# Optimization experiments

Measured on AMD Instinct MI355X. Metric: run time of the kernel, lower is better.

## Reference

```python
import jax, jax.numpy as jnp
import numpy as np

# Static config (matches init_kwargs / spatial layout)
SHAPES = ((64, 64), (32, 32), (16, 16))   # (H, W) per level, bev=256 at /4,/8,/16
B, HEADS, LEVELS, POINTS, C = 2, 8, 3, 4, 256
HD = C // HEADS
NV = sum(h * w for h, w in SHAPES)        # 5376
NQ = NV
TP = HEADS * LEVELS * POINTS              # 96


def setup_inputs() -> dict:
    key = jax.random.key(0)
    ks = jax.random.split(key, 10)
    s = 1.0 / np.sqrt(C)
    inp = {
        'query': jax.random.normal(ks[0], (B, NQ, C), dtype=jnp.float32),
        'reference_points': jax.random.uniform(ks[1], (B, NQ, 2), dtype=jnp.float32),
        'value': jax.random.normal(ks[2], (B, NV, C), dtype=jnp.float32),
        'Wv': jax.random.normal(ks[3], (C, C), dtype=jnp.float32) * s,
        'bv': jnp.zeros((C,), dtype=jnp.float32),
        # offset proj: small scale so sampling stays local-ish (orig init is 0)
        'Woff': jax.random.normal(ks[4], (TP * 2, C), dtype=jnp.float32) * (0.02 * s),
        'boff': jnp.zeros((TP * 2,), dtype=jnp.float32),
        'Wa': jax.random.normal(ks[5], (TP, C), dtype=jnp.float32) * s,
        'ba': jnp.zeros((TP,), dtype=jnp.float32),
        'Wo': jax.random.normal(ks[6], (C, C), dtype=jnp.float32) * s,
        'bo': jnp.zeros((C,), dtype=jnp.float32),
    }
    return inp


def _msda(query, reference_points, value, Wv, bv, Woff, boff, Wa, ba, Wo, bo):
    Bb, nq, _ = query.shape
    # value projection -> per-head values
    v = (value @ Wv.T + bv).reshape(Bb, NV, HEADS, HD)
    # sampling offsets: (B, NQ, HEADS, LEVELS, POINTS, 2)
    off = (query @ Woff.T + boff).reshape(Bb, nq, HEADS, LEVELS, POINTS, 2)
    # attention weights: softmax over LEVELS*POINTS jointly
    a = (query @ Wa.T + ba).reshape(Bb, nq, HEADS, LEVELS * POINTS)
    a = jax.nn.softmax(a, axis=-1).reshape(Bb, nq, HEADS, LEVELS, POINTS)
    # sampling locations in [0,1] (clamp matches torch .clamp(0,1))
    loc = jnp.clip(reference_points[:, :, None, None, None, :] + off, 0.0, 1.0)

    out = jnp.zeros((Bb, HEADS, nq, HD), dtype=query.dtype)
    start = 0
    for lvl, (H, W) in enumerate(SHAPES):
        n = H * W
        # (B, HEADS, H*W, HD) flattened level feature map per head
        vl = jnp.transpose(v[:, start:start + n].reshape(Bb, H, W, HEADS, HD),
                           (0, 3, 1, 2, 4)).reshape(Bb, HEADS, n, HD)
        loc_l = loc[:, :, :, lvl]                     # (B, NQ, HEADS, K, 2)
        # align_corners=False unnormalization: ((g+1)*size - 1)/2 with g=2*loc-1
        x = loc_l[..., 0] * W - 0.5
        y = loc_l[..., 1] * H - 0.5
        x0 = jnp.floor(x)
        y0 = jnp.floor(y)
        wx1 = x - x0
        wy1 = y - y0
        x0i = x0.astype(jnp.int32)
        y0i = y0.astype(jnp.int32)
        acc = jnp.zeros((Bb, HEADS, nq * POINTS, HD), dtype=query.dtype)
        for dy in (0, 1):
            for dx in (0, 1):
                ix = x0i + dx
                iy = y0i + dy
                wgt = (wx1 if dx else 1.0 - wx1) * (wy1 if dy else 1.0 - wy1)
                # zero padding outside the map (padding_mode='zeros')
                valid = (ix >= 0) & (ix < W) & (iy >= 0) & (iy < H)
                idx = jnp.clip(iy, 0, H - 1) * W + jnp.clip(ix, 0, W - 1)
                idx_t = jnp.transpose(idx, (0, 2, 1, 3)).reshape(Bb, HEADS, nq * POINTS)
                g = jnp.take_along_axis(vl, idx_t[..., None], axis=2)  # (B,H,NQ*K,HD)
                w_t = jnp.transpose(wgt * valid.astype(wgt.dtype),
                                    (0, 2, 1, 3)).reshape(Bb, HEADS, nq * POINTS, 1)
                acc = acc + g * w_t
        aw = jnp.transpose(a[:, :, :, lvl], (0, 2, 1, 3)).reshape(Bb, HEADS, nq * POINTS, 1)
        out = out + (acc * aw).reshape(Bb, HEADS, nq, POINTS, HD).sum(axis=3)
        start += n
    out = jnp.transpose(out, (0, 2, 1, 3)).reshape(Bb, nq, C)
    return out @ Wo.T + bo


def reference(query, reference_points, value, Wv, bv, Woff, boff, Wa, ba, Wo, bo):
    return _msda(query, reference_points, value, Wv, bv, Woff, boff, Wa, ba, Wo, bo)
```

## Files before the change

kernel.cpp:

```cpp
#include <hip/hip_runtime.h>
#include <hip/hip_bf16.h>
#include <cmath>

#define BATCH   2
#define NQ      5376
#define NV      5376
#define CDIM    256
#define HEADS   8
#define HD      32
#define LEVELS  3
#define POINTS  4
#define TP      96
#define MROWS   (BATCH*NQ)
#define NOFF    (TP*2)
#define NQA     (NOFF+TP)

typedef __attribute__((ext_vector_type(8))) short bf16x8;
typedef __attribute__((ext_vector_type(4))) float f32x4;
typedef unsigned short u16;
typedef unsigned int   u32;

#define AS1 __attribute__((address_space(1)))
#define AS3 __attribute__((address_space(3)))

__device__ __forceinline__ void g2lds16(const void* g, void* l) {
    __builtin_amdgcn_global_load_lds((const AS1 void*)g, (AS3 void*)l, 16, 0, 0);
}

__device__ __forceinline__ u16 bf_of(float f) {
    union { __hip_bfloat16 h; u16 s; } u;
    u.h = __float2bfloat16(f);
    return u.s;
}
__device__ __forceinline__ float bf_back(u16 s) {
    return __uint_as_float((u32)s << 16);
}

__device__ __forceinline__ ushort4 cvt_hi(float4 v) {
    ushort4 h;
    h.x = bf_of(v.x); h.y = bf_of(v.y); h.z = bf_of(v.z); h.w = bf_of(v.w);
    return h;
}
__device__ __forceinline__ ushort4 cvt_lo(float4 v, ushort4 h) {
    ushort4 l;
    l.x = bf_of(v.x - bf_back(h.x));
    l.y = bf_of(v.y - bf_back(h.y));
    l.z = bf_of(v.z - bf_back(h.z));
    l.w = bf_of(v.w - bf_back(h.w));
    return l;
}

#define GBM 64
#define GBN 64
#define GBK 32

#define VBLOCKS (168 * 4)
__global__ __launch_bounds__(256) void gemm_vqa_kernel(
    const float* __restrict__ value, const float* __restrict__ Wv,
    const float* __restrict__ bv, u16* __restrict__ vOut,
    const float* __restrict__ query, const float* __restrict__ Woff,
    const float* __restrict__ Wa,
    const float* __restrict__ boff, const float* __restrict__ ba,
    u16* __restrict__ offOut, u16* __restrict__ aOut)
{
    __shared__ u16 sAh[GBM * GBK];
    __shared__ u16 sAl[GBM * GBK];
    __shared__ u16 sBh[GBN * GBK];

    const int bid = blockIdx.x;
    const bool vpath = bid < VBLOCKS;
    int m0, n0;
    if (vpath) { m0 = (bid >> 2) * GBM;           n0 = (bid & 3) * GBN; }
    else       { const int b2 = bid - VBLOCKS;
                 m0 = (b2 / 5) * GBM;             n0 = (b2 % 5) * GBN; }

    const int tid  = threadIdx.x;
    const int lane = tid & 63;
    const int wave = tid >> 6;
    const int wr   = wave & 1;
    const int wc   = wave >> 1;
    const int qm   = lane & 15;
    const int quad = lane >> 4;

    const int srow = tid >> 2;
    const int sc   = (tid & 3) * 8;

    const float* Asrc = (vpath ? value : query) + (size_t)(m0 + srow) * CDIM;
    const float* Bsrc;
    if (vpath) {
        Bsrc = Wv + (size_t)(n0 + srow) * CDIM;
    } else {
        const int rg = min(n0 + srow, NQA - 1);
        Bsrc = (rg < NOFF) ? (Woff + (size_t)rg * CDIM)
                           : (Wa + (size_t)(rg - NOFF) * CDIM);
    }

    f32x4 acc[2][2];
    #pragma unroll
    for (int i = 0; i < 2; ++i)
        #pragma unroll
        for (int j = 0; j < 2; ++j)
            acc[i][j] = (f32x4){0.f, 0.f, 0.f, 0.f};

    for (int k0 = 0; k0 < CDIM; k0 += GBK) {
        const float4 a0 = *reinterpret_cast<const float4*>(&Asrc[k0 + sc]);
        const float4 a1 = *reinterpret_cast<const float4*>(&Asrc[k0 + sc + 4]);
        const ushort4 ah0 = cvt_hi(a0), ah1 = cvt_hi(a1);
        *reinterpret_cast<ushort4*>(&sAh[srow * GBK + sc])     = ah0;
        *reinterpret_cast<ushort4*>(&sAh[srow * GBK + sc + 4]) = ah1;
        if (vpath) {
            *reinterpret_cast<ushort4*>(&sAl[srow * GBK + sc])     = cvt_lo(a0, ah0);
            *reinterpret_cast<ushort4*>(&sAl[srow * GBK + sc + 4]) = cvt_lo(a1, ah1);
        }
        const float4 b0 = *reinterpret_cast<const float4*>(&Bsrc[k0 + sc]);
        const float4 b1 = *reinterpret_cast<const float4*>(&Bsrc[k0 + sc + 4]);
        *reinterpret_cast<ushort4*>(&sBh[srow * GBK + sc])     = cvt_hi(b0);
        *reinterpret_cast<ushort4*>(&sBh[srow * GBK + sc + 4]) = cvt_hi(b1);
        __syncthreads();

        bf16x8 fah[2], fal[2], fbh[2];
        #pragma unroll
        for (int x = 0; x < 2; ++x) {
            const int rm = wr * 32 + x * 16 + qm;
            const int rn = wc * 32 + x * 16 + qm;
            fah[x] = *reinterpret_cast<const bf16x8*>(&sAh[rm * GBK + quad * 8]);
            fbh[x] = *reinterpret_cast<const bf16x8*>(&sBh[rn * GBK + quad * 8]);
            if (vpath)
                fal[x] = *reinterpret_cast<const bf16x8*>(&sAl[rm * GBK + quad * 8]);
        }
        #pragma unroll
        for (int mi = 0; mi < 2; ++mi)
            #pragma unroll
            for (int ni = 0; ni < 2; ++ni) {
                acc[mi][ni] = __builtin_amdgcn_mfma_f32_16x16x32_bf16(
                    fah[mi], fbh[ni], acc[mi][ni], 0, 0, 0);
                if (vpath)
                    acc[mi][ni] = __builtin_amdgcn_mfma_f32_16x16x32_bf16(
                        fal[mi], fbh[ni], acc[mi][ni], 0, 0, 0);
            }
        __syncthreads();
    }

    #pragma unroll
    for (int mi = 0; mi < 2; ++mi) {
        #pragma unroll
        for (int ni = 0; ni < 2; ++ni) {
            const int n = n0 + wc * 32 + ni * 16 + qm;
            if (vpath) {
                const float bn = bv[n];
                #pragma unroll
                for (int r = 0; r < 4; ++r) {
                    const int m = m0 + wr * 32 + mi * 16 + quad * 4 + r;
                    const float val = acc[mi][ni][r] + bn;
                    const int b = m / NV, rr = m - b * NV;
                    const int h = n >> 5, c = n & 31;
                    vOut[(((size_t)b * HEADS + h) * NV + rr) * HD + c] = bf_of(val);
                }
            } else {
                if (n >= NQA) continue;
                const float bn = (n < NOFF) ? boff[n] : ba[n - NOFF];
                #pragma unroll
                for (int r = 0; r < 4; ++r) {
                    const int m = m0 + wr * 32 + mi * 16 + quad * 4 + r;
                    const float val = acc[mi][ni][r] + bn;
                    if (n < NOFF)
                        offOut[(size_t)m * NOFF + n] = bf_of(val);
                    else
                        aOut[(size_t)m * TP + (n - NOFF)] = bf_of(val);
                }
            }
        }
    }
}

__global__ __launch_bounds__(256) void gemm_out_kernel(
    const u16* __restrict__ Ah,
    const float* __restrict__ Wo, const float* __restrict__ bias,
    float* __restrict__ Cout)
{
    __shared__ u16 sAh[GBM * GBK];
    __shared__ u16 sBh[GBN * GBK];

    const int bid = blockIdx.x;
    const int m0 = (bid >> 2) * GBM;
    const int n0 = (bid & 3) * GBN;

    const int tid  = threadIdx.x;
    const int lane = tid & 63;
    const int wave = tid >> 6;
    const int wr   = wave & 1;
    const int wc   = wave >> 1;
    const int qm   = lane & 15;
    const int quad = lane >> 4;

    const int arow = (wave << 4) + (lane >> 2);
    const int ak   = (lane & 3) * 8;
    const int srow = tid >> 2;
    const int sc   = (tid & 3) * 8;
    const float* Bsrc = Wo + (size_t)(n0 + srow) * CDIM;

    f32x4 acc[2][2];
    #pragma unroll
    for (int i = 0; i < 2; ++i)
        #pragma unroll
        for (int j = 0; j < 2; ++j)
            acc[i][j] = (f32x4){0.f, 0.f, 0.f, 0.f};

    for (int k0 = 0; k0 < CDIM; k0 += GBK) {
        const size_t ga = (size_t)(m0 + arow) * CDIM + k0 + ak;
        g2lds16(Ah + ga, sAh + wave * 512);
        const float4 b0 = *reinterpret_cast<const float4*>(&Bsrc[k0 + sc]);
        const float4 b1 = *reinterpret_cast<const float4*>(&Bsrc[k0 + sc + 4]);
        *reinterpret_cast<ushort4*>(&sBh[srow * GBK + sc])     = cvt_hi(b0);
        *reinterpret_cast<ushort4*>(&sBh[srow * GBK + sc + 4]) = cvt_hi(b1);
        __syncthreads();

        bf16x8 fah[2], fbh[2];
        #pragma unroll
        for (int x = 0; x < 2; ++x) {
            const int rm = wr * 32 + x * 16 + qm;
            const int rn = wc * 32 + x * 16 + qm;
            fah[x] = *reinterpret_cast<const bf16x8*>(&sAh[rm * GBK + quad * 8]);
            fbh[x] = *reinterpret_cast<const bf16x8*>(&sBh[rn * GBK + quad * 8]);
        }
        #pragma unroll
        for (int mi = 0; mi < 2; ++mi)
            #pragma unroll
            for (int ni = 0; ni < 2; ++ni)
                acc[mi][ni] = __builtin_amdgcn_mfma_f32_16x16x32_bf16(
                    fah[mi], fbh[ni], acc[mi][ni], 0, 0, 0);
        __syncthreads();
    }

    #pragma unroll
    for (int mi = 0; mi < 2; ++mi) {
        #pragma unroll
        for (int ni = 0; ni < 2; ++ni) {
            const int n = n0 + wc * 32 + ni * 16 + qm;
            const float bn = bias[n];
            #pragma unroll
            for (int r = 0; r < 4; ++r) {
                const int m = m0 + wr * 32 + mi * 16 + quad * 4 + r;
                Cout[(size_t)m * CDIM + n] = acc[mi][ni][r] + bn;
            }
        }
    }
}

__global__ __launch_bounds__(256) void msda_core_kernel(
    const u16* __restrict__ off,
    const u16* __restrict__ alog,
    const float* __restrict__ refp,
    const u16*   __restrict__ v,
    u16* __restrict__ t_hi)
{
    const int tid = threadIdx.x;
    const int bq0 = blockIdx.x * 4;

    __shared__ float s_w[4][TP];
    __shared__ int   s_idx[4][TP][4];
    __shared__ float s_twt[4][TP][4];

    #pragma unroll
    for (int base = 0; base < 4 * TP; base += 256) {
        const int idx = base + tid;
        if (idx < 4 * TP) {
            const int q = idx / TP, j = idx - q * TP;
            s_w[q][j] = bf_back(alog[(size_t)(bq0 + q) * TP + j]);
        }
    }
    __syncthreads();

    if (tid < 32) {
        const int q = tid >> 3, h = tid & 7;
        float mx = -1e30f;
        #pragma unroll
        for (int i = 0; i < 12; ++i) mx = fmaxf(mx, s_w[q][h * 12 + i]);
        float e[12];
        float sum = 0.f;
        #pragma unroll
        for (int i = 0; i < 12; ++i) {
            e[i] = expf(s_w[q][h * 12 + i] - mx);
            sum += e[i];
        }
        const float inv = 1.f / sum;
        #pragma unroll
        for (int i = 0; i < 12; ++i) s_w[q][h * 12 + i] = e[i] * inv;
    }
    __syncthreads();

    #pragma unroll
    for (int base = 0; base < 4 * TP; base += 256) {
        const int idx = base + tid;
        if (idx < 4 * TP) {
            const int q = idx / TP, j = idx - q * TP;
            const int bq = bq0 + q;
            const int jj = j % 12;
            const int l  = jj >> 2;
            const int Wl    = (l == 0) ? 64 : (l == 1) ? 32 : 16;
            const int start = (l == 0) ? 0 : (l == 1) ? 4096 : 5120;

            const float refx = refp[(size_t)bq * 2 + 0];
            const float refy = refp[(size_t)bq * 2 + 1];
            const float ox = bf_back(off[(size_t)bq * NOFF + j * 2 + 0]);
            const float oy = bf_back(off[(size_t)bq * NOFF + j * 2 + 1]);
            const float lx = fminf(fmaxf(refx + ox, 0.f), 1.f) * (float)Wl - 0.5f;
            const float ly = fminf(fmaxf(refy + oy, 0.f), 1.f) * (float)Wl - 0.5f;
            const float fx0 = floorf(lx), fy0 = floorf(ly);
            const int   x0  = (int)fx0,   y0  = (int)fy0;
            const float wx1 = lx - fx0,   wy1 = ly - fy0;
            const float wx0 = 1.f - wx1,  wy0 = 1.f - wy1;
            const float aw  = s_w[q][j];

            #pragma unroll
            for (int k = 0; k < 4; ++k) {
                const int dx = k & 1, dy = k >> 1;
                const int xi = x0 + dx, yi = y0 + dy;
                const bool ok = (xi >= 0) & (xi < Wl) & (yi >= 0) & (yi < Wl);
                const int xc = min(max(xi, 0), Wl - 1);
                const int yc = min(max(yi, 0), Wl - 1);
                s_idx[q][j][k] = (start + yc * Wl + xc) * (HD * 2);
                const float wxy = (dx ? wx1 : wx0) * (dy ? wy1 : wy0);
                s_twt[q][j][k] = ok ? aw * wxy : 0.f;
            }
        }
    }
    __syncthreads();

    const int qsel = tid >> 6;
    const int ht   = tid & 63;
    const int h    = ht >> 3;
    const int sub  = ht & 7;
    const int oct  = sub & 3;
    const int rep  = sub >> 2;
    const int bq   = bq0 + qsel;
    const int b    = bq / NQ;
    const char* vb = (const char*)v + (((size_t)b * HEADS + h) * NV) * (HD * 2) + oct * 16;

    float acc[8] = {};
    #pragma unroll
    for (int g = 0; g < 3; ++g) {
        uint4 raw[8];
        float wt[8];
        #pragma unroll
        for (int pp = 0; pp < 2; ++pp) {
            const int j = h * 12 + rep * 6 + g * 2 + pp;
            const int4   ix = *reinterpret_cast<const int4*>(&s_idx[qsel][j][0]);
            const float4 tw = *reinterpret_cast<const float4*>(&s_twt[qsel][j][0]);
            raw[pp * 4 + 0] = *reinterpret_cast<const uint4*>(vb + ix.x);
            raw[pp * 4 + 1] = *reinterpret_cast<const uint4*>(vb + ix.y);
            raw[pp * 4 + 2] = *reinterpret_cast<const uint4*>(vb + ix.z);
            raw[pp * 4 + 3] = *reinterpret_cast<const uint4*>(vb + ix.w);
            wt[pp * 4 + 0] = tw.x; wt[pp * 4 + 1] = tw.y;
            wt[pp * 4 + 2] = tw.z; wt[pp * 4 + 3] = tw.w;
        }
        #pragma unroll
        for (int k = 0; k < 8; ++k) {
            acc[0] += wt[k] * __uint_as_float(raw[k].x << 16);
            acc[1] += wt[k] * __uint_as_float(raw[k].x & 0xffff0000u);
            acc[2] += wt[k] * __uint_as_float(raw[k].y << 16);
            acc[3] += wt[k] * __uint_as_float(raw[k].y & 0xffff0000u);
            acc[4] += wt[k] * __uint_as_float(raw[k].z << 16);
            acc[5] += wt[k] * __uint_as_float(raw[k].z & 0xffff0000u);
            acc[6] += wt[k] * __uint_as_float(raw[k].w << 16);
            acc[7] += wt[k] * __uint_as_float(raw[k].w & 0xffff0000u);
        }
    }

    #pragma unroll
    for (int c = 0; c < 8; ++c)
        acc[c] += __shfl_xor(acc[c], 4);

    if (rep == 0) {
        uint4 o;
        o.x = (u32)bf_of(acc[0]) | ((u32)bf_of(acc[1]) << 16);
        o.y = (u32)bf_of(acc[2]) | ((u32)bf_of(acc[3]) << 16);
        o.z = (u32)bf_of(acc[4]) | ((u32)bf_of(acc[5]) << 16);
        o.w = (u32)bf_of(acc[6]) | ((u32)bf_of(acc[7]) << 16);
        const size_t base = (size_t)bq * CDIM + h * HD + oct * 8;
        *reinterpret_cast<uint4*>(t_hi + base) = o;
    }
}

extern "C" void kernel_launch(void* const* d_in, const int* in_sizes, int n_in,
                              void* d_out, int out_size, void* d_ws, size_t ws_size,
                              hipStream_t stream)
{
    const float* query = (const float*)d_in[0];
    const float* refp  = (const float*)d_in[1];
    const float* value = (const float*)d_in[2];
    const float* Wv    = (const float*)d_in[3];
    const float* bv    = (const float*)d_in[4];
    const float* Woff  = (const float*)d_in[5];
    const float* boff  = (const float*)d_in[6];
    const float* Wa    = (const float*)d_in[7];
    const float* ba    = (const float*)d_in[8];
    const float* Wo    = (const float*)d_in[9];
    const float* bo    = (const float*)d_in[10];
    float* out = (float*)d_out;

    char* w = (char*)d_ws;
    const size_t SZ_T = (size_t)MROWS * CDIM * 2;
    u16* v_bf16 = (u16*)(w);
    u16* t_hi   = (u16*)(w + 1 * SZ_T);
    u16* ws_off = (u16*)(w + 2 * SZ_T);
    u16* ws_a   = (u16*)(w + 2 * SZ_T + (size_t)MROWS * NOFF * 2);

    const dim3 blk(256);

    gemm_vqa_kernel<<<dim3(VBLOCKS + (MROWS / GBM) * 5), blk, 0, stream>>>(
        value, Wv, bv, v_bf16,
        query, Woff, Wa, boff, ba, ws_off, ws_a);

    msda_core_kernel<<<dim3(MROWS / 4), blk, 0, stream>>>(
        ws_off, ws_a, refp, v_bf16, t_hi);

    gemm_out_kernel<<<dim3((MROWS / GBM) * 4), blk, 0, stream>>>(
        t_hi, Wo, bo, out);
}
```

Before: 135.0 us.

## Pre-convert inputs to bf16 and double-buffer GEMM tiles via direct LDS loads

Adds a prep kernel that converts value (hi/lo split), query and all weight matrices to bf16 in the workspace, and pads the combined offset/attention weight to 320 rows. Both GEMM kernels then load tiles with global_load_lds into double-buffered shared memory, prefetching the next K slice while computing the current one. Block indices are also remapped across 8 groups, apparently to spread work across the chip's XCDs. This removes in-loop fp32 conversion and one barrier per K step, at the cost of an extra launch and a full extra pass writing and re-reading the bf16 copies of value and query.

Result: no change. 134.4 us (-0.4%).

```diff
diff --git a/kernel.cpp b/kernel.cpp
--- a/kernel.cpp
+++ b/kernel.cpp
@@ -14,6 +14,7 @@
 #define MROWS   (BATCH*NQ)
 #define NOFF    (TP*2)
 #define NQA     (NOFF+TP)
+#define NQAP    320
 
 typedef __attribute__((ext_vector_type(8))) short bf16x8;
 typedef __attribute__((ext_vector_type(4))) float f32x4;
@@ -50,29 +51,110 @@
     return l;
 }
 
+#define NVAL8  344064
+#define NQRY8  344064
+#define NWV8   8192
+#define NWOFF8 6144
+#define NWA8   3072
+#define NWO8   8192
+#define NPAD8  1024
+#define PREP_BLOCKS 2792
+__global__ __launch_bounds__(256) void prep_kernel(
+    const float* __restrict__ value, const float* __restrict__ query,
+    const float* __restrict__ Wv, const float* __restrict__ Woff,
+    const float* __restrict__ Wa, const float* __restrict__ Wo,
+    u16* __restrict__ val_hi, u16* __restrict__ val_lo,
+    u16* __restrict__ q_hi, u16* __restrict__ wv_h,
+    u16* __restrict__ wqa_h, u16* __restrict__ wo_h)
+{
+    int r = blockIdx.x * 256 + threadIdx.x;
+
+    if (r < NVAL8) {
+        const float4 a0 = *reinterpret_cast<const float4*>(value + (size_t)r * 8);
+        const float4 a1 = *reinterpret_cast<const float4*>(value + (size_t)r * 8 + 4);
+        const ushort4 h0 = cvt_hi(a0), h1 = cvt_hi(a1);
+        *reinterpret_cast<ushort4*>(val_hi + (size_t)r * 8)     = h0;
+        *reinterpret_cast<ushort4*>(val_hi + (size_t)r * 8 + 4) = h1;
+        *reinterpret_cast<ushort4*>(val_lo + (size_t)r * 8)     = cvt_lo(a0, h0);
+        *reinterpret_cast<ushort4*>(val_lo + (size_t)r * 8 + 4) = cvt_lo(a1, h1);
+        return;
+    }
+    r -= NVAL8;
+    if (r < NQRY8) {
+        const float4 a0 = *reinterpret_cast<const float4*>(query + (size_t)r * 8);
+        const float4 a1 = *reinterpret_cast<const float4*>(query + (size_t)r * 8 + 4);
+        *reinterpret_cast<ushort4*>(q_hi + (size_t)r * 8)     = cvt_hi(a0);
+        *reinterpret_cast<ushort4*>(q_hi + (size_t)r * 8 + 4) = cvt_hi(a1);
+        return;
+    }
+    r -= NQRY8;
+    if (r < NWV8) {
+        const float4 a0 = *reinterpret_cast<const float4*>(Wv + (size_t)r * 8);
+        const float4 a1 = *reinterpret_cast<const float4*>(Wv + (size_t)r * 8 + 4);
+        *reinterpret_cast<ushort4*>(wv_h + (size_t)r * 8)     = cvt_hi(a0);
+        *reinterpret_cast<ushort4*>(wv_h + (size_t)r * 8 + 4) = cvt_hi(a1);
+        return;
+    }
+    r -= NWV8;
+    if (r < NWOFF8) {
+        const float4 a0 = *reinterpret_cast<const float4*>(Woff + (size_t)r * 8);
+        const float4 a1 = *reinterpret_cast<const float4*>(Woff + (size_t)r * 8 + 4);
+        *reinterpret_cast<ushort4*>(wqa_h + (size_t)r * 8)     = cvt_hi(a0);
+        *reinterpret_cast<ushort4*>(wqa_h + (size_t)r * 8 + 4) = cvt_hi(a1);
+        return;
+    }
+    r -= NWOFF8;
+    if (r < NWA8) {
+        const float4 a0 = *reinterpret_cast<const float4*>(Wa + (size_t)r * 8);
+        const float4 a1 = *reinterpret_cast<const float4*>(Wa + (size_t)r * 8 + 4);
+        u16* dst = wqa_h + (size_t)NOFF * CDIM;
+        *reinterpret_cast<ushort4*>(dst + (size_t)r * 8)     = cvt_hi(a0);
+        *reinterpret_cast<ushort4*>(dst + (size_t)r * 8 + 4) = cvt_hi(a1);
+        return;
+    }
+    r -= NWA8;
+    if (r < NWO8) {
+        const float4 a0 = *reinterpret_cast<const float4*>(Wo + (size_t)r * 8);
+        const float4 a1 = *reinterpret_cast<const float4*>(Wo + (size_t)r * 8 + 4);
+        *reinterpret_cast<ushort4*>(wo_h + (size_t)r * 8)     = cvt_hi(a0);
+        *reinterpret_cast<ushort4*>(wo_h + (size_t)r * 8 + 4) = cvt_hi(a1);
+        return;
+    }
+    r -= NWO8;
+    const ushort4 z = {0, 0, 0, 0};
+    u16* dst = wqa_h + (size_t)NQA * CDIM;
+    *reinterpret_cast<ushort4*>(dst + (size_t)r * 8)     = z;
+    *reinterpret_cast<ushort4*>(dst + (size_t)r * 8 + 4) = z;
+}
+
 #define GBM 64
 #define GBN 64
 #define GBK 32
 
 #define VBLOCKS (168 * 4)
+#define K1_BLOCKS (VBLOCKS + 168 * 5)
+#define K1_CPX (K1_BLOCKS / 8)
+
 __global__ __launch_bounds__(256) void gemm_vqa_kernel(
-    const float* __restrict__ value, const float* __restrict__ Wv,
-    const float* __restrict__ bv, u16* __restrict__ vOut,
-    const float* __restrict__ query, const float* __restrict__ Woff,
-    const float* __restrict__ Wa,
-    const float* __restrict__ boff, const float* __restrict__ ba,
-    u16* __restrict__ offOut, u16* __restrict__ aOut)
+    const u16* __restrict__ val_hi, const u16* __restrict__ val_lo,
+    const u16* __restrict__ q_hi,
+    const u16* __restrict__ wv_h, const u16* __restrict__ wqa_h,
+    const float* __restrict__ bv, const float* __restrict__ boff,
+    const float* __restrict__ ba,
+    u16* __restrict__ vOut, u16* __restrict__ offOut, u16* __restrict__ aOut)
 {
-    __shared__ u16 sAh[GBM * GBK];
-    __shared__ u16 sAl[GBM * GBK];
-    __shared__ u16 sBh[GBN * GBK];
-
-    const int bid = blockIdx.x;
+    __shared__ __align__(16) u16 sAh[2][GBM * GBK];
+    __shared__ __align__(16) u16 sAl[2][GBM * GBK];
+    __shared__ __align__(16) u16 sBh[2][GBM * GBK];
+
+    const int bid0 = blockIdx.x;
+    const int bid = (bid0 & 7) * K1_CPX + (bid0 >> 3);
+
     const bool vpath = bid < VBLOCKS;
     int m0, n0;
-    if (vpath) { m0 = (bid >> 2) * GBM;           n0 = (bid & 3) * GBN; }
+    if (vpath) { m0 = (bid >> 2) * GBM;          n0 = (bid & 3) * GBM; }
     else       { const int b2 = bid - VBLOCKS;
-                 m0 = (b2 / 5) * GBM;             n0 = (b2 % 5) * GBN; }
+                 m0 = (b2 / 5) * GBM;            n0 = (b2 % 5) * GBM; }
 
     const int tid  = threadIdx.x;
     const int lane = tid & 63;
@@ -82,18 +164,12 @@
     const int qm   = lane & 15;
     const int quad = lane >> 4;
 
-    const int srow = tid >> 2;
-    const int sc   = (tid & 3) * 8;
-
-    const float* Asrc = (vpath ? value : query) + (size_t)(m0 + srow) * CDIM;
-    const float* Bsrc;
-    if (vpath) {
-        Bsrc = Wv + (size_t)(n0 + srow) * CDIM;
-    } else {
-        const int rg = min(n0 + srow, NQA - 1);
-        Bsrc = (rg < NOFF) ? (Woff + (size_t)rg * CDIM)
-                           : (Wa + (size_t)(rg - NOFF) * CDIM);
-    }
+    const int arow = (wave << 4) + (lane >> 2);
+    const int ak   = (lane & 3) * 8;
+
+    const u16* Asrc_h = (vpath ? val_hi : q_hi) + (size_t)(m0 + arow) * CDIM + ak;
+    const u16* Asrc_l = val_lo + (size_t)(m0 + arow) * CDIM + ak;
+    const u16* Bsrc   = (vpath ? wv_h : wqa_h) + (size_t)(n0 + arow) * CDIM + ak;
 
     f32x4 acc[2][2];
     #pragma unroll
@@ -102,31 +178,30 @@
         for (int j = 0; j < 2; ++j)
             acc[i][j] = (f32x4){0.f, 0.f, 0.f, 0.f};
 
+    {
+        g2lds16(Asrc_h, &sAh[0][wave * 512]);
+        if (vpath) g2lds16(Asrc_l, &sAl[0][wave * 512]);
+        g2lds16(Bsrc, &sBh[0][wave * 512]);
+    }
+    __syncthreads();
+
+    int cur = 0;
     for (int k0 = 0; k0 < CDIM; k0 += GBK) {
-        const float4 a0 = *reinterpret_cast<const float4*>(&Asrc[k0 + sc]);
-        const float4 a1 = *reinterpret_cast<const float4*>(&Asrc[k0 + sc + 4]);
-        const ushort4 ah0 = cvt_hi(a0), ah1 = cvt_hi(a1);
-        *reinterpret_cast<ushort4*>(&sAh[srow * GBK + sc])     = ah0;
-        *reinterpret_cast<ushort4*>(&sAh[srow * GBK + sc + 4]) = ah1;
-        if (vpath) {
-            *reinterpret_cast<ushort4*>(&sAl[srow * GBK + sc])     = cvt_lo(a0, ah0);
-            *reinterpret_cast<ushort4*>(&sAl[srow * GBK + sc + 4]) = cvt_lo(a1, ah1);
-        }
-        const float4 b0 = *reinterpret_cast<const float4*>(&Bsrc[k0 + sc]);
-        const float4 b1 = *reinterpret_cast<const float4*>(&Bsrc[k0 + sc + 4]);
-        *reinterpret_cast<ushort4*>(&sBh[srow * GBK + sc])     = cvt_hi(b0);
-        *reinterpret_cast<ushort4*>(&sBh[srow * GBK + sc + 4]) = cvt_hi(b1);
-        __syncthreads();
+        if (k0 + GBK < CDIM) {
+            g2lds16(Asrc_h + k0 + GBK, &sAh[cur ^ 1][wave * 512]);
+            if (vpath) g2lds16(Asrc_l + k0 + GBK, &sAl[cur ^ 1][wave * 512]);
+            g2lds16(Bsrc + k0 + GBK, &sBh[cur ^ 1][wave * 512]);
+        }
 
         bf16x8 fah[2], fal[2], fbh[2];
         #pragma unroll
         for (int x = 0; x < 2; ++x) {
             const int rm = wr * 32 + x * 16 + qm;
             const int rn = wc * 32 + x * 16 + qm;
-            fah[x] = *reinterpret_cast<const bf16x8*>(&sAh[rm * GBK + quad * 8]);
-            fbh[x] = *reinterpret_cast<const bf16x8*>(&sBh[rn * GBK + quad * 8]);
+            fah[x] = *reinterpret_cast<const bf16x8*>(&sAh[cur][rm * GBK + quad * 8]);
+            fbh[x] = *reinterpret_cast<const bf16x8*>(&sBh[cur][rn * GBK + quad * 8]);
             if (vpath)
-                fal[x] = *reinterpret_cast<const bf16x8*>(&sAl[rm * GBK + quad * 8]);
+                fal[x] = *reinterpret_cast<const bf16x8*>(&sAl[cur][rm * GBK + quad * 8]);
         }
         #pragma unroll
         for (int mi = 0; mi < 2; ++mi)
@@ -139,6 +214,7 @@
                         fal[mi], fbh[ni], acc[mi][ni], 0, 0, 0);
             }
         __syncthreads();
+        cur ^= 1;
     }
 
     #pragma unroll
@@ -173,17 +249,20 @@
     }
 }
 
+#define K3_BLOCKS ((MROWS / GBM) * 4)
+#define K3_CPX (K3_BLOCKS / 8)
+
 __global__ __launch_bounds__(256) void gemm_out_kernel(
-    const u16* __restrict__ Ah,
-    const float* __restrict__ Wo, const float* __restrict__ bias,
-    float* __restrict__ Cout)
+    const u16* __restrict__ Ah, const u16* __restrict__ wo_h,
+    const float* __restrict__ bias, float* __restrict__ Cout)
 {
-    __shared__ u16 sAh[GBM * GBK];
-    __shared__ u16 sBh[GBN * GBK];
-
-    const int bid = blockIdx.x;
+    __shared__ __align__(16) u16 sAh[2][GBM * GBK];
+    __shared__ __align__(16) u16 sBh[2][GBM * GBK];
+
+    const int bid0 = blockIdx.x;
+    const int bid = (bid0 & 7) * K3_CPX + (bid0 >> 3);
     const int m0 = (bid >> 2) * GBM;
-    const int n0 = (bid & 3) * GBN;
+    const int n0 = (bid & 3) * GBM;
 
     const int tid  = threadIdx.x;
     const int lane = tid & 63;
@@ -195,9 +274,9 @@
 
     const int arow = (wave << 4) + (lane >> 2);
     const int ak   = (lane & 3) * 8;
-    const int srow = tid >> 2;
-    const int sc   = (tid & 3) * 8;
-    const float* Bsrc = Wo + (size_t)(n0 + srow) * CDIM;
+
+    const u16* Asrc = Ah   + (size_t)(m0 + arow) * CDIM + ak;
+    const u16* Bsrc = wo_h + (size_t)(n0 + arow) * CDIM + ak;
 
     f32x4 acc[2][2];
     #pragma unroll
@@ -206,22 +285,24 @@
         for (int j = 0; j < 2; ++j)
             acc[i][j] = (f32x4){0.f, 0.f, 0.f, 0.f};
 
+    g2lds16(Asrc, &sAh[0][wave * 512]);
+    g2lds16(Bsrc, &sBh[0][wave * 512]);
+    __syncthreads();
+
+    int cur = 0;
     for (int k0 = 0; k0 < CDIM; k0 += GBK) {
-        const size_t ga = (size_t)(m0 + arow) * CDIM + k0 + ak;
-        g2lds16(Ah + ga, sAh + wave * 512);
-        const float4 b0 = *reinterpret_cast<const float4*>(&Bsrc[k0 + sc]);
-        const float4 b1 = *reinterpret_cast<const float4*>(&Bsrc[k0 + sc + 4]);
-        *reinterpret_cast<ushort4*>(&sBh[srow * GBK + sc])     = cvt_hi(b0);
-        *reinterpret_cast<ushort4*>(&sBh[srow * GBK + sc + 4]) = cvt_hi(b1);
-        __syncthreads();
+        if (k0 + GBK < CDIM) {
+            g2lds16(Asrc + k0 + GBK, &sAh[cur ^ 1][wave * 512]);
+            g2lds16(Bsrc + k0 + GBK, &sBh[cur ^ 1][wave * 512]);
+        }
 
         bf16x8 fah[2], fbh[2];
         #pragma unroll
         for (int x = 0; x < 2; ++x) {
             const int rm = wr * 32 + x * 16 + qm;
             const int rn = wc * 32 + x * 16 + qm;
-            fah[x] = *reinterpret_cast<const bf16x8*>(&sAh[rm * GBK + quad * 8]);
-            fbh[x] = *reinterpret_cast<const bf16x8*>(&sBh[rn * GBK + quad * 8]);
+            fah[x] = *reinterpret_cast<const bf16x8*>(&sAh[cur][rm * GBK + quad * 8]);
+            fbh[x] = *reinterpret_cast<const bf16x8*>(&sBh[cur][rn * GBK + quad * 8]);
         }
         #pragma unroll
         for (int mi = 0; mi < 2; ++mi)
@@ -230,6 +311,7 @@
                 acc[mi][ni] = __builtin_amdgcn_mfma_f32_16x16x32_bf16(
                     fah[mi], fbh[ni], acc[mi][ni], 0, 0, 0);
         __syncthreads();
+        cur ^= 1;
     }
 
     #pragma unroll
@@ -405,16 +487,28 @@
     u16* t_hi   = (u16*)(w + 1 * SZ_T);
     u16* ws_off = (u16*)(w + 2 * SZ_T);
     u16* ws_a   = (u16*)(w + 2 * SZ_T + (size_t)MROWS * NOFF * 2);
+    char* w2    = w + 2 * SZ_T + (size_t)MROWS * NQA * 2;
+    u16* val_hi = (u16*)(w2);
+    u16* val_lo = (u16*)(w2 + 1 * SZ_T);
+    u16* q_hi   = (u16*)(w2 + 2 * SZ_T);
+    u16* wv_h   = (u16*)(w2 + 3 * SZ_T);
+    u16* wqa_h  = (u16*)(w2 + 3 * SZ_T + (size_t)CDIM * CDIM * 2);
+    u16* wo_h   = (u16*)(w2 + 3 * SZ_T + (size_t)CDIM * CDIM * 2
+                              + (size_t)NQAP * CDIM * 2);
 
     const dim3 blk(256);
 
-    gemm_vqa_kernel<<<dim3(VBLOCKS + (MROWS / GBM) * 5), blk, 0, stream>>>(
-        value, Wv, bv, v_bf16,
-        query, Woff, Wa, boff, ba, ws_off, ws_a);
+    prep_kernel<<<dim3(PREP_BLOCKS), blk, 0, stream>>>(
+        value, query, Wv, Woff, Wa, Wo,
+        val_hi, val_lo, q_hi, wv_h, wqa_h, wo_h);
+
+    gemm_vqa_kernel<<<dim3(K1_BLOCKS), blk, 0, stream>>>(
+        val_hi, val_lo, q_hi, wv_h, wqa_h,
+        bv, boff, ba, v_bf16, ws_off, ws_a);
 
     msda_core_kernel<<<dim3(MROWS / 4), blk, 0, stream>>>(
         ws_off, ws_a, refp, v_bf16, t_hi);
 
-    gemm_out_kernel<<<dim3((MROWS / GBM) * 4), blk, 0, stream>>>(
-        t_hi, Wo, bo, out);
-}
+    gemm_out_kernel<<<dim3(K3_BLOCKS), blk, 0, stream>>>(
+        t_hi, wo_h, bo, out);
+}
```

## Fuse output projection into MSDA sampling kernel and pre-convert Wo to bf16

Applied to the files above, without the earlier changes.

Merges the sampling/aggregation kernel with the output projection GEMM. Each 512-thread block handles 16 queries, stages the aggregated rows in LDS, and multiplies them by a bf16 copy of Wo using MFMA. This removes the intermediate write and read of the aggregated tensor and one kernel launch. The first kernel also converts Wo to bf16, pads its LDS rows to avoid bank conflicts, and swizzles block indices across XCDs. Softmax is computed per wave, with normalization applied after accumulation. In exchange, the fused kernel uses larger blocks with more LDS, and Wo is reread from global/L2 by every block.

After: 131.5 us. 1.03x faster.

```diff
diff --git a/kernel.cpp b/kernel.cpp
--- a/kernel.cpp
+++ b/kernel.cpp
@@ -20,13 +20,6 @@
 typedef unsigned short u16;
 typedef unsigned int   u32;
 
-#define AS1 __attribute__((address_space(1)))
-#define AS3 __attribute__((address_space(3)))
-
-__device__ __forceinline__ void g2lds16(const void* g, void* l) {
-    __builtin_amdgcn_global_load_lds((const AS1 void*)g, (AS3 void*)l, 16, 0, 0);
-}
-
 __device__ __forceinline__ u16 bf_of(float f) {
     union { __hip_bfloat16 h; u16 s; } u;
     u.h = __float2bfloat16(f);
@@ -35,7 +28,6 @@
 __device__ __forceinline__ float bf_back(u16 s) {
     return __uint_as_float((u32)s << 16);
 }
-
 __device__ __forceinline__ ushort4 cvt_hi(float4 v) {
     ushort4 h;
     h.x = bf_of(v.x); h.y = bf_of(v.y); h.z = bf_of(v.z); h.w = bf_of(v.w);
@@ -53,28 +45,44 @@
 #define GBM 64
 #define GBN 64
 #define GBK 32
+#define SAP 40
 
 #define VBLOCKS (168 * 4)
-__global__ __launch_bounds__(256) void gemm_vqa_kernel(
+#define K1_BLOCKS (VBLOCKS + 168 * 5)
+#define K1_CPX (K1_BLOCKS / 8)
+
+__global__ __launch_bounds__(256) void gemm_vqa_conv(
     const float* __restrict__ value, const float* __restrict__ Wv,
     const float* __restrict__ bv, u16* __restrict__ vOut,
     const float* __restrict__ query, const float* __restrict__ Woff,
     const float* __restrict__ Wa,
     const float* __restrict__ boff, const float* __restrict__ ba,
-    u16* __restrict__ offOut, u16* __restrict__ aOut)
+    u16* __restrict__ offOut, u16* __restrict__ aOut,
+    const float* __restrict__ Wo, u16* __restrict__ wo_h)
 {
-    __shared__ u16 sAh[GBM * GBK];
-    __shared__ u16 sAl[GBM * GBK];
-    __shared__ u16 sBh[GBN * GBK];
-
-    const int bid = blockIdx.x;
+    __shared__ __align__(16) u16 sAh[GBM * SAP];
+    __shared__ __align__(16) u16 sAl[GBM * SAP];
+    __shared__ __align__(16) u16 sBh[GBM * SAP];
+
+    const int bid0 = blockIdx.x;
+    const int tid  = threadIdx.x;
+
+    if (bid0 < 32) {
+        const int e = bid0 * 2048 + tid * 8;
+        const float4 a0 = *reinterpret_cast<const float4*>(Wo + e);
+        const float4 a1 = *reinterpret_cast<const float4*>(Wo + e + 4);
+        *reinterpret_cast<ushort4*>(wo_h + e)     = cvt_hi(a0);
+        *reinterpret_cast<ushort4*>(wo_h + e + 4) = cvt_hi(a1);
+    }
+
+    const int bid = (bid0 & 7) * K1_CPX + (bid0 >> 3);
+
     const bool vpath = bid < VBLOCKS;
     int m0, n0;
-    if (vpath) { m0 = (bid >> 2) * GBM;           n0 = (bid & 3) * GBN; }
+    if (vpath) { m0 = (bid >> 2) * GBM;          n0 = (bid & 3) * GBN; }
     else       { const int b2 = bid - VBLOCKS;
-                 m0 = (b2 / 5) * GBM;             n0 = (b2 % 5) * GBN; }
-
-    const int tid  = threadIdx.x;
+                 m0 = (b2 / 5) * GBM;            n0 = (b2 % 5) * GBN; }
+
     const int lane = tid & 63;
     const int wave = tid >> 6;
     const int wr   = wave & 1;
@@ -106,16 +114,16 @@
         const float4 a0 = *reinterpret_cast<const float4*>(&Asrc[k0 + sc]);
         const float4 a1 = *reinterpret_cast<const float4*>(&Asrc[k0 + sc + 4]);
         const ushort4 ah0 = cvt_hi(a0), ah1 = cvt_hi(a1);
-        *reinterpret_cast<ushort4*>(&sAh[srow * GBK + sc])     = ah0;
-        *reinterpret_cast<ushort4*>(&sAh[srow * GBK + sc + 4]) = ah1;
+        *reinterpret_cast<ushort4*>(&sAh[srow * SAP + sc])     = ah0;
+        *reinterpret_cast<ushort4*>(&sAh[srow * SAP + sc + 4]) = ah1;
         if (vpath) {
-            *reinterpret_cast<ushort4*>(&sAl[srow * GBK + sc])     = cvt_lo(a0, ah0);
-            *reinterpret_cast<ushort4*>(&sAl[srow * GBK + sc + 4]) = cvt_lo(a1, ah1);
+            *reinterpret_cast<ushort4*>(&sAl[srow * SAP + sc])     = cvt_lo(a0, ah0);
+            *reinterpret_cast<ushort4*>(&sAl[srow * SAP + sc + 4]) = cvt_lo(a1, ah1);
         }
         const float4 b0 = *reinterpret_cast<const float4*>(&Bsrc[k0 + sc]);
         const float4 b1 = *reinterpret_cast<const float4*>(&Bsrc[k0 + sc + 4]);
-        *reinterpret_cast<ushort4*>(&sBh[srow * GBK + sc])     = cvt_hi(b0);
-        *reinterpret_cast<ushort4*>(&sBh[srow * GBK + sc + 4]) = cvt_hi(b1);
+        *reinterpret_cast<ushort4*>(&sBh[srow * SAP + sc])     = cvt_hi(b0);
+        *reinterpret_cast<ushort4*>(&sBh[srow * SAP + sc + 4]) = cvt_hi(b1);
         __syncthreads();
 
         bf16x8 fah[2], fal[2], fbh[2];
@@ -123,10 +131,10 @@
         for (int x = 0; x < 2; ++x) {
             const int rm = wr * 32 + x * 16 + qm;
             const int rn = wc * 32 + x * 16 + qm;
-            fah[x] = *reinterpret_cast<const bf16x8*>(&sAh[rm * GBK + quad * 8]);
-            fbh[x] = *reinterpret_cast<const bf16x8*>(&sBh[rn * GBK + quad * 8]);
+            fah[x] = *reinterpret_cast<const bf16x8*>(&sAh[rm * SAP + quad * 8]);
+            fbh[x] = *reinterpret_cast<const bf16x8*>(&sBh[rn * SAP + quad * 8]);
             if (vpath)
-                fal[x] = *reinterpret_cast<const bf16x8*>(&sAl[rm * GBK + quad * 8]);
+                fal[x] = *reinterpret_cast<const bf16x8*>(&sAl[rm * SAP + quad * 8]);
         }
         #pragma unroll
         for (int mi = 0; mi < 2; ++mi)
@@ -173,212 +181,206 @@
     }
 }
 
-__global__ __launch_bounds__(256) void gemm_out_kernel(
-    const u16* __restrict__ Ah,
-    const float* __restrict__ Wo, const float* __restrict__ bias,
-    float* __restrict__ Cout)
-{
-    __shared__ u16 sAh[GBM * GBK];
-    __shared__ u16 sBh[GBN * GBK];
-
-    const int bid = blockIdx.x;
-    const int m0 = (bid >> 2) * GBM;
-    const int n0 = (bid & 3) * GBN;
-
-    const int tid  = threadIdx.x;
-    const int lane = tid & 63;
-    const int wave = tid >> 6;
-    const int wr   = wave & 1;
-    const int wc   = wave >> 1;
-    const int qm   = lane & 15;
-    const int quad = lane >> 4;
-
-    const int arow = (wave << 4) + (lane >> 2);
-    const int ak   = (lane & 3) * 8;
-    const int srow = tid >> 2;
-    const int sc   = (tid & 3) * 8;
-    const float* Bsrc = Wo + (size_t)(n0 + srow) * CDIM;
-
-    f32x4 acc[2][2];
-    #pragma unroll
-    for (int i = 0; i < 2; ++i)
-        #pragma unroll
-        for (int j = 0; j < 2; ++j)
-            acc[i][j] = (f32x4){0.f, 0.f, 0.f, 0.f};
-
-    for (int k0 = 0; k0 < CDIM; k0 += GBK) {
-        const size_t ga = (size_t)(m0 + arow) * CDIM + k0 + ak;
-        g2lds16(Ah + ga, sAh + wave * 512);
-        const float4 b0 = *reinterpret_cast<const float4*>(&Bsrc[k0 + sc]);
-        const float4 b1 = *reinterpret_cast<const float4*>(&Bsrc[k0 + sc + 4]);
-        *reinterpret_cast<ushort4*>(&sBh[srow * GBK + sc])     = cvt_hi(b0);
-        *reinterpret_cast<ushort4*>(&sBh[srow * GBK + sc + 4]) = cvt_hi(b1);
-        __syncthreads();
-
-        bf16x8 fah[2], fbh[2];
-        #pragma unroll
-        for (int x = 0; x < 2; ++x) {
-            const int rm = wr * 32 + x * 16 + qm;
-            const int rn = wc * 32 + x * 16 + qm;
-            fah[x] = *reinterpret_cast<const bf16x8*>(&sAh[rm * GBK + quad * 8]);
-            fbh[x] = *reinterpret_cast<const bf16x8*>(&sBh[rn * GBK + quad * 8]);
-        }
-        #pragma unroll
-        for (int mi = 0; mi < 2; ++mi)
-            #pragma unroll
-            for (int ni = 0; ni < 2; ++ni)
-                acc[mi][ni] = __builtin_amdgcn_mfma_f32_16x16x32_bf16(
-                    fah[mi], fbh[ni], acc[mi][ni], 0, 0, 0);
-        __syncthreads();
-    }
-
-    #pragma unroll
-    for (int mi = 0; mi < 2; ++mi) {
-        #pragma unroll
-        for (int ni = 0; ni < 2; ++ni) {
-            const int n = n0 + wc * 32 + ni * 16 + qm;
-            const float bn = bias[n];
-            #pragma unroll
-            for (int r = 0; r < 4; ++r) {
-                const int m = m0 + wr * 32 + mi * 16 + quad * 4 + r;
-                Cout[(size_t)m * CDIM + n] = acc[mi][ni][r] + bn;
-            }
-        }
-    }
-}
-
-__global__ __launch_bounds__(256) void msda_core_kernel(
+#define MSDA_SLAB 3584
+#define QPB 16
+#define K2_BLOCKS (MROWS / QPB)
+#define K2_CPX (K2_BLOCKS / 8)
+#define TSTR 264
+
+__global__ __launch_bounds__(512) void msda_out_kernel(
     const u16* __restrict__ off,
     const u16* __restrict__ alog,
     const float* __restrict__ refp,
     const u16*   __restrict__ v,
-    u16* __restrict__ t_hi)
+    const u16*   __restrict__ wo_h,
+    const float* __restrict__ bo,
+    float* __restrict__ out)
 {
-    const int tid = threadIdx.x;
-    const int bq0 = blockIdx.x * 4;
-
-    __shared__ float s_w[4][TP];
-    __shared__ int   s_idx[4][TP][4];
-    __shared__ float s_twt[4][TP][4];
+    __shared__ __align__(16) char slabs[8 * MSDA_SLAB];
+    __shared__ __align__(16) u16  t_lds[QPB * TSTR];
+
+    const int tid  = threadIdx.x;
+    const int wave = tid >> 6;
+    const int lane = tid & 63;
+
+    const int bid0 = blockIdx.x;
+    const int bid  = (bid0 & 7) * K2_CPX + (bid0 >> 3);
+    const int bq0  = bid * QPB;
+
+    char* slab = slabs + wave * MSDA_SLAB;
+    float* s_w   = reinterpret_cast<float*>(slab);
+    float* s_mx  = reinterpret_cast<float*>(slab + 384);
+    float* s_inv = reinterpret_cast<float*>(slab + 416);
+    int*   s_idx = reinterpret_cast<int*>  (slab + 448);
+    float* s_twt = reinterpret_cast<float*>(slab + 1984);
+
+    const int h   = lane >> 3;
+    const int sub = lane & 7;
+    const int oct = sub & 3;
+    const int rep = sub >> 2;
 
     #pragma unroll
-    for (int base = 0; base < 4 * TP; base += 256) {
-        const int idx = base + tid;
-        if (idx < 4 * TP) {
-            const int q = idx / TP, j = idx - q * TP;
-            s_w[q][j] = bf_back(alog[(size_t)(bq0 + q) * TP + j]);
-        }
-    }
+    for (int iter = 0; iter < 2; ++iter) {
+        const int r  = iter * 8 + wave;
+        const int bq = bq0 + r;
+        const int b  = bq / NQ;
+
+        if (lane < 12) {
+            const bf16x8 lg = *reinterpret_cast<const bf16x8*>(
+                &alog[(size_t)bq * TP + lane * 8]);
+            float4 f0, f1;
+            f0.x = bf_back((u16)lg[0]); f0.y = bf_back((u16)lg[1]);
+            f0.z = bf_back((u16)lg[2]); f0.w = bf_back((u16)lg[3]);
+            f1.x = bf_back((u16)lg[4]); f1.y = bf_back((u16)lg[5]);
+            f1.z = bf_back((u16)lg[6]); f1.w = bf_back((u16)lg[7]);
+            *reinterpret_cast<float4*>(&s_w[lane * 8])     = f0;
+            *reinterpret_cast<float4*>(&s_w[lane * 8 + 4]) = f1;
+        }
+
+        if (lane < 8) {
+            const float4 a = *reinterpret_cast<const float4*>(&s_w[lane * 12]);
+            const float4 c = *reinterpret_cast<const float4*>(&s_w[lane * 12 + 4]);
+            const float4 d = *reinterpret_cast<const float4*>(&s_w[lane * 12 + 8]);
+            s_mx[lane] = fmaxf(
+                fmaxf(fmaxf(a.x, a.y), fmaxf(a.z, a.w)),
+                fmaxf(fmaxf(fmaxf(c.x, c.y), fmaxf(c.z, c.w)),
+                      fmaxf(fmaxf(d.x, d.y), fmaxf(d.z, d.w))));
+        }
+
+        const float refx = refp[(size_t)bq * 2 + 0];
+        const float refy = refp[(size_t)bq * 2 + 1];
+        #pragma unroll
+        for (int half = 0; half < 2; ++half) {
+            const int j = half * 64 + lane;
+            if (half == 0 || lane < 32) {
+                const int jj = j % 12;
+                const int l  = jj >> 2;
+                const int Wl    = (l == 0) ? 64 : (l == 1) ? 32 : 16;
+                const int start = (l == 0) ? 0 : (l == 1) ? 4096 : 5120;
+
+                const u32 o2 = *reinterpret_cast<const u32*>(
+                    &off[(size_t)bq * NOFF + j * 2]);
+                const float ox = bf_back((u16)(o2 & 0xffffu));
+                const float oy = bf_back((u16)(o2 >> 16));
+                const float aw = expf(s_w[j] - s_mx[j / 12]);
+
+                const float lx = fminf(fmaxf(refx + ox, 0.f), 1.f) * (float)Wl - 0.5f;
+                const float ly = fminf(fmaxf(refy + oy, 0.f), 1.f) * (float)Wl - 0.5f;
+                const float fx0 = floorf(lx), fy0 = floorf(ly);
+                const int   x0  = (int)fx0,   y0  = (int)fy0;
+                const float wx1 = lx - fx0,   wy1 = ly - fy0;
+                const float wx0 = 1.f - wx1,  wy0 = 1.f - wy1;
+
+                int   idv[4];
+                float twv[4];
+                #pragma unroll
+                for (int k = 0; k < 4; ++k) {
+                    const int dx = k & 1, dy = k >> 1;
+                    const int xi = x0 + dx, yi = y0 + dy;
+                    const bool ok = (xi >= 0) & (xi < Wl) & (yi >= 0) & (yi < Wl);
+                    const int xc = min(max(xi, 0), Wl - 1);
+                    const int yc = min(max(yi, 0), Wl - 1);
+                    idv[k] = (start + yc * Wl + xc) * (HD * 2);
+                    const float wxy = (dx ? wx1 : wx0) * (dy ? wy1 : wy0);
+                    twv[k] = ok ? aw * wxy : 0.f;
+                }
+                int4 id; id.x = idv[0]; id.y = idv[1]; id.z = idv[2]; id.w = idv[3];
+                float4 tw; tw.x = twv[0]; tw.y = twv[1]; tw.z = twv[2]; tw.w = twv[3];
+                *reinterpret_cast<int4*>(&s_idx[j * 4])   = id;
+                *reinterpret_cast<float4*>(&s_twt[j * 4]) = tw;
+                s_w[j] = aw;
+            }
+        }
+
+        if (lane < 8) {
+            const float4 a = *reinterpret_cast<const float4*>(&s_w[lane * 12]);
+            const float4 c = *reinterpret_cast<const float4*>(&s_w[lane * 12 + 4]);
+            const float4 d = *reinterpret_cast<const float4*>(&s_w[lane * 12 + 8]);
+            s_inv[lane] = 1.f / (((a.x + a.y) + (a.z + a.w))
+                               + ((c.x + c.y) + (c.z + c.w))
+                               + ((d.x + d.y) + (d.z + d.w)));
+        }
+
+        const char* vb = (const char*)v
+            + (((size_t)b * HEADS + h) * NV) * (HD * 2) + oct * 16;
+
+        float acc[8] = {};
+        #pragma unroll
+        for (int g = 0; g < 3; ++g) {
+            uint4 raw[8];
+            float wt[8];
+            #pragma unroll
+            for (int pp = 0; pp < 2; ++pp) {
+                const int j = h * 12 + rep * 6 + g * 2 + pp;
+                const int4   ix = *reinterpret_cast<const int4*>(&s_idx[j * 4]);
+                const float4 tw = *reinterpret_cast<const float4*>(&s_twt[j * 4]);
+                raw[pp * 4 + 0] = *reinterpret_cast<const uint4*>(vb + ix.x);
+                raw[pp * 4 + 1] = *reinterpret_cast<const uint4*>(vb + ix.y);
+                raw[pp * 4 + 2] = *reinterpret_cast<const uint4*>(vb + ix.z);
+                raw[pp * 4 + 3] = *reinterpret_cast<const uint4*>(vb + ix.w);
+                wt[pp * 4 + 0] = tw.x; wt[pp * 4 + 1] = tw.y;
+                wt[pp * 4 + 2] = tw.z; wt[pp * 4 + 3] = tw.w;
+            }
+            #pragma unroll
+            for (int k = 0; k < 8; ++k) {
+                acc[0] += wt[k] * __uint_as_float(raw[k].x << 16);
+                acc[1] += wt[k] * __uint_as_float(raw[k].x & 0xffff0000u);
+                acc[2] += wt[k] * __uint_as_float(raw[k].y << 16);
+                acc[3] += wt[k] * __uint_as_float(raw[k].y & 0xffff0000u);
+                acc[4] += wt[k] * __uint_as_float(raw[k].z << 16);
+                acc[5] += wt[k] * __uint_as_float(raw[k].z & 0xffff0000u);
+                acc[6] += wt[k] * __uint_as_float(raw[k].w << 16);
+                acc[7] += wt[k] * __uint_as_float(raw[k].w & 0xffff0000u);
+            }
+        }
+
+        const float inv = s_inv[h];
+        #pragma unroll
+        for (int c = 0; c < 8; ++c)
+            acc[c] = (acc[c] + __shfl_xor(acc[c], 4)) * inv;
+
+        if (rep == 0) {
+            uint4 o;
+            o.x = (u32)bf_of(acc[0]) | ((u32)bf_of(acc[1]) << 16);
+            o.y = (u32)bf_of(acc[2]) | ((u32)bf_of(acc[3]) << 16);
+            o.z = (u32)bf_of(acc[4]) | ((u32)bf_of(acc[5]) << 16);
+            o.w = (u32)bf_of(acc[6]) | ((u32)bf_of(acc[7]) << 16);
+            *reinterpret_cast<uint4*>(&t_lds[r * TSTR + h * HD + oct * 8]) = o;
+        }
+    }
+
     __syncthreads();
 
-    if (tid < 32) {
-        const int q = tid >> 3, h = tid & 7;
-        float mx = -1e30f;
-        #pragma unroll
-        for (int i = 0; i < 12; ++i) mx = fmaxf(mx, s_w[q][h * 12 + i]);
-        float e[12];
-        float sum = 0.f;
-        #pragma unroll
-        for (int i = 0; i < 12; ++i) {
-            e[i] = expf(s_w[q][h * 12 + i] - mx);
-            sum += e[i];
-        }
-        const float inv = 1.f / sum;
-        #pragma unroll
-        for (int i = 0; i < 12; ++i) s_w[q][h * 12 + i] = e[i] * inv;
-    }
-    __syncthreads();
+    const int qm   = lane & 15;
+    const int quad = lane >> 4;
+
+    f32x4 acc2[2];
+    acc2[0] = (f32x4){0.f, 0.f, 0.f, 0.f};
+    acc2[1] = (f32x4){0.f, 0.f, 0.f, 0.f};
 
     #pragma unroll
-    for (int base = 0; base < 4 * TP; base += 256) {
-        const int idx = base + tid;
-        if (idx < 4 * TP) {
-            const int q = idx / TP, j = idx - q * TP;
-            const int bq = bq0 + q;
-            const int jj = j % 12;
-            const int l  = jj >> 2;
-            const int Wl    = (l == 0) ? 64 : (l == 1) ? 32 : 16;
-            const int start = (l == 0) ? 0 : (l == 1) ? 4096 : 5120;
-
-            const float refx = refp[(size_t)bq * 2 + 0];
-            const float refy = refp[(size_t)bq * 2 + 1];
-            const float ox = bf_back(off[(size_t)bq * NOFF + j * 2 + 0]);
-            const float oy = bf_back(off[(size_t)bq * NOFF + j * 2 + 1]);
-            const float lx = fminf(fmaxf(refx + ox, 0.f), 1.f) * (float)Wl - 0.5f;
-            const float ly = fminf(fmaxf(refy + oy, 0.f), 1.f) * (float)Wl - 0.5f;
-            const float fx0 = floorf(lx), fy0 = floorf(ly);
-            const int   x0  = (int)fx0,   y0  = (int)fy0;
-            const float wx1 = lx - fx0,   wy1 = ly - fy0;
-            const float wx0 = 1.f - wx1,  wy0 = 1.f - wy1;
-            const float aw  = s_w[q][j];
-
-            #pragma unroll
-            for (int k = 0; k < 4; ++k) {
-                const int dx = k & 1, dy = k >> 1;
-                const int xi = x0 + dx, yi = y0 + dy;
-                const bool ok = (xi >= 0) & (xi < Wl) & (yi >= 0) & (yi < Wl);
-                const int xc = min(max(xi, 0), Wl - 1);
-                const int yc = min(max(yi, 0), Wl - 1);
-                s_idx[q][j][k] = (start + yc * Wl + xc) * (HD * 2);
-                const float wxy = (dx ? wx1 : wx0) * (dy ? wy1 : wy0);
-                s_twt[q][j][k] = ok ? aw * wxy : 0.f;
-            }
-        }
-    }
-    __syncthreads();
-
-    const int qsel = tid >> 6;
-    const int ht   = tid & 63;
-    const int h    = ht >> 3;
-    const int sub  = ht & 7;
-    const int oct  = sub & 3;
-    const int rep  = sub >> 2;
-    const int bq   = bq0 + qsel;
-    const int b    = bq / NQ;
-    const char* vb = (const char*)v + (((size_t)b * HEADS + h) * NV) * (HD * 2) + oct * 16;
-
-    float acc[8] = {};
+    for (int k0 = 0; k0 < CDIM; k0 += 32) {
+        const bf16x8 fa = *reinterpret_cast<const bf16x8*>(
+            &t_lds[qm * TSTR + k0 + quad * 8]);
+        #pragma unroll
+        for (int ni = 0; ni < 2; ++ni) {
+            const int rn = wave * 32 + ni * 16 + qm;
+            const bf16x8 fb = *reinterpret_cast<const bf16x8*>(
+                &wo_h[(size_t)rn * CDIM + k0 + quad * 8]);
+            acc2[ni] = __builtin_amdgcn_mfma_f32_16x16x32_bf16(
+                fa, fb, acc2[ni], 0, 0, 0);
+        }
+    }
+
     #pragma unroll
-    for (int g = 0; g < 3; ++g) {
-        uint4 raw[8];
-        float wt[8];
-        #pragma unroll
-        for (int pp = 0; pp < 2; ++pp) {
-            const int j = h * 12 + rep * 6 + g * 2 + pp;
-            const int4   ix = *reinterpret_cast<const int4*>(&s_idx[qsel][j][0]);
-            const float4 tw = *reinterpret_cast<const float4*>(&s_twt[qsel][j][0]);
-            raw[pp * 4 + 0] = *reinterpret_cast<const uint4*>(vb + ix.x);
-            raw[pp * 4 + 1] = *reinterpret_cast<const uint4*>(vb + ix.y);
-            raw[pp * 4 + 2] = *reinterpret_cast<const uint4*>(vb + ix.z);
-            raw[pp * 4 + 3] = *reinterpret_cast<const uint4*>(vb + ix.w);
-            wt[pp * 4 + 0] = tw.x; wt[pp * 4 + 1] = tw.y;
-            wt[pp * 4 + 2] = tw.z; wt[pp * 4 + 3] = tw.w;
-        }
-        #pragma unroll
-        for (int k = 0; k < 8; ++k) {
-            acc[0] += wt[k] * __uint_as_float(raw[k].x << 16);
-            acc[1] += wt[k] * __uint_as_float(raw[k].x & 0xffff0000u);
-            acc[2] += wt[k] * __uint_as_float(raw[k].y << 16);
-            acc[3] += wt[k] * __uint_as_float(raw[k].y & 0xffff0000u);
-            acc[4] += wt[k] * __uint_as_float(raw[k].z << 16);
-            acc[5] += wt[k] * __uint_as_float(raw[k].z & 0xffff0000u);
-            acc[6] += wt[k] * __uint_as_float(raw[k].w << 16);
-            acc[7] += wt[k] * __uint_as_float(raw[k].w & 0xffff0000u);
-        }
-    }
-
-    #pragma unroll
-    for (int c = 0; c < 8; ++c)
-        acc[c] += __shfl_xor(acc[c], 4);
-
-    if (rep == 0) {
-        uint4 o;
-        o.x = (u32)bf_of(acc[0]) | ((u32)bf_of(acc[1]) << 16);
-        o.y = (u32)bf_of(acc[2]) | ((u32)bf_of(acc[3]) << 16);
-        o.z = (u32)bf_of(acc[4]) | ((u32)bf_of(acc[5]) << 16);
-        o.w = (u32)bf_of(acc[6]) | ((u32)bf_of(acc[7]) << 16);
-        const size_t base = (size_t)bq * CDIM + h * HD + oct * 8;
-        *reinterpret_cast<uint4*>(t_hi + base) = o;
+    for (int ni = 0; ni < 2; ++ni) {
+        const int n  = wave * 32 + ni * 16 + qm;
+        const float bn = bo[n];
+        #pragma unroll
+        for (int r = 0; r < 4; ++r) {
+            const int m = bq0 + quad * 4 + r;
+            out[(size_t)m * CDIM + n] = acc2[ni][r] + bn;
+        }
     }
 }
 
@@ -402,19 +404,17 @@
     char* w = (char*)d_ws;
     const size_t SZ_T = (size_t)MROWS * CDIM * 2;
     u16* v_bf16 = (u16*)(w);
-    u16* t_hi   = (u16*)(w + 1 * SZ_T);
-    u16* ws_off = (u16*)(w + 2 * SZ_T);
-    u16* ws_a   = (u16*)(w + 2 * SZ_T + (size_t)MROWS * NOFF * 2);
+    u16* ws_off = (u16*)(w + 1 * SZ_T);
+    u16* ws_a   = (u16*)(w + 1 * SZ_T + (size_t)MROWS * NOFF * 2);
+    u16* wo_h   = (u16*)(w + 1 * SZ_T + (size_t)MROWS * NQA * 2);
 
     const dim3 blk(256);
 
-    gemm_vqa_kernel<<<dim3(VBLOCKS + (MROWS / GBM) * 5), blk, 0, stream>>>(
+    gemm_vqa_conv<<<dim3(K1_BLOCKS), blk, 0, stream>>>(
         value, Wv, bv, v_bf16,
-        query, Woff, Wa, boff, ba, ws_off, ws_a);
-
-    msda_core_kernel<<<dim3(MROWS / 4), blk, 0, stream>>>(
-        ws_off, ws_a, refp, v_bf16, t_hi);
-
-    gemm_out_kernel<<<dim3((MROWS / GBM) * 4), blk, 0, stream>>>(
-        t_hi, Wo, bo, out);
-}
+        query, Woff, Wa, boff, ba, ws_off, ws_a,
+        Wo, wo_h);
+
+    msda_out_kernel<<<dim3(K2_BLOCKS), dim3(512), 0, stream>>>(
+        ws_off, ws_a, refp, v_bf16, wo_h, bo, out);
+}
```
